# Kernel optimization log

Hardware: AMD Instinct MI355X
Metric: run time of the kernel (lower is better)

The kernel has to match this reference:

```python
import jax, jax.numpy as jnp
import numpy as np

B, L, DIM, S, K = 2, 2048, 1024, 16, 3
INNER = DIM  # expand = 1 (module only runs with expand=1, see notes)


def setup_inputs() -> dict:
    key = jax.random.key(0)
    ks = jax.random.split(key, 10)
    f = lambda k, shape, s=0.02: jax.random.normal(k, shape, jnp.float32) * s
    return {
        "x": jax.random.normal(ks[0], (B, L, DIM), jnp.float32),
        "gamma": jnp.ones((DIM,), jnp.float32),
        "beta": jnp.zeros((DIM,), jnp.float32),
        "W_in": f(ks[1], (2 * INNER, DIM)),
        "conv_w": f(ks[2], (INNER, 1, K), 0.2),   # depthwise conv, OIL layout
        "W_x": f(ks[3], (2 * S, INNER)),
        "W_dt": f(ks[4], (INNER, DIM)),
        "b_dt": f(ks[5], (INNER,), 0.1),
        "A_log": jax.random.normal(ks[6], (INNER, S), jnp.float32),
        "D_param": jnp.ones((INNER,), jnp.float32),
        "W_out": f(ks[7], (DIM, INNER)),
    }


def reference(x, gamma, beta, W_in, conv_w, W_x, W_dt, b_dt, A_log, D_param, W_out):
    residual = x
    # LayerNorm
    mu = jnp.mean(x, axis=-1, keepdims=True)
    var = jnp.var(x, axis=-1, keepdims=True)
    h = (x - mu) / jnp.sqrt(var + 1e-5) * gamma + beta
    # in_proj + chunk
    xz = jnp.einsum('bld,ed->ble', h, W_in)
    inner = W_in.shape[0] // 2
    xx, z = xz[..., :inner], xz[..., inner:]
    # depthwise conv1d, padding (K-1)//2, no bias
    k = conv_w.shape[-1]
    pad = (k - 1) // 2
    xc = jax.lax.conv_general_dilated(
        xx.transpose(0, 2, 1), conv_w, window_strides=(1,),
        padding=[(pad, pad)], dimension_numbers=('NCL', 'OIL', 'NCL'),
        feature_group_count=inner).transpose(0, 2, 1)
    xc = jax.nn.silu(xc)
    # projections for dt, B, C
    dt = jnp.einsum('bld,ed->ble', xc, W_dt) + b_dt
    BC = jnp.einsum('bld,ed->ble', xc, W_x)
    s = A_log.shape[-1]
    Bm, Cm = BC[..., :s], BC[..., s:]
    # selective scan
    A = -jnp.exp(A_log)                               # (d, s)
    dt = jax.nn.softplus(dt)                          # (b, l, d)
    dA = jnp.exp(jnp.einsum('bld,ds->blds', dt, A))   # (b, l, d, s)
    dB = jnp.einsum('bld,bls->blds', dt, Bm)          # (b, l, d, s)

    def step(state, inputs):
        dA_t, dB_t, C_t = inputs                      # (b,d,s), (b,d,s), (b,s)
        state = state * dA_t + dB_t
        y_t = jnp.einsum('bds,bs->bd', state, C_t)
        return state, y_t

    init = jnp.zeros((x.shape[0], inner, s), xc.dtype)
    _, ys = jax.lax.scan(
        step, init,
        (dA.transpose(1, 0, 2, 3), dB.transpose(1, 0, 2, 3), Cm.transpose(1, 0, 2)))
    y = ys.transpose(1, 0, 2)                         # (b, l, d)
    # skip, gate, out projection, residual
    y = y + D_param * xc
    y = y * jax.nn.silu(z)
    out = jnp.einsum('bld,ed->ble', y, W_out)
    return out + residual
```

## Files before the change

### kernel.cpp

```cpp
#include <hip/hip_runtime.h>
#include <math.h>

#define BB 2
#define LL 2048
#define DIMV 1024
#define SSV 16
#define INNERV 1024
#define E2V 2048
#define MMV (BB*LL)
#define NCHUNK 64
#define CLEN 32

typedef __attribute__((ext_vector_type(8))) short short8;
typedef __attribute__((ext_vector_type(4))) float f32x4;

static __device__ __forceinline__ float4 ld4(const float* p){
  return *reinterpret_cast<const float4*>(p);
}
static __device__ __forceinline__ ushort f2bf(float x){
  unsigned u = __float_as_uint(x);
  unsigned r = (u + 0x7fffu + ((u >> 16) & 1u)) >> 16;
  return (ushort)r;
}
static __device__ __forceinline__ float bf2f(ushort h){
  return __uint_as_float(((unsigned)h) << 16);
}
static __device__ __forceinline__ void gld16(const void* g, void* l){
  __builtin_amdgcn_global_load_lds(
      (const __attribute__((address_space(1))) void*)g,
      (__attribute__((address_space(3))) void*)l, 16, 0, 0);
}

__global__ __launch_bounds__(256) void ln_init(
        const float* __restrict__ x, const float* __restrict__ gamma,
        const float* __restrict__ beta, ushort* __restrict__ hh,
        const float* __restrict__ W_in, const float* __restrict__ W_dt,
        const float* __restrict__ W_out, const float* __restrict__ wx,
        ushort* __restrict__ Wih, ushort* __restrict__ Wdh,
        ushort* __restrict__ Woh, float* __restrict__ wxt){
  __shared__ float red[8];
  if (blockIdx.x < 4224){
    int idx = blockIdx.x*256 + threadIdx.x;
    if (idx < 1024*1024){
      const float* src; ushort* dst; int i;
      if (idx < 512*1024){ src = W_in;  dst = Wih; i = idx; }
      else if (idx < 768*1024){ src = W_dt;  dst = Wdh; i = idx - 512*1024; }
      else { src = W_out; dst = Woh; i = idx - 768*1024; }
      float4 v = ld4(src + (size_t)i*4);
      ushort4 H;
      H.x=f2bf(v.x); H.y=f2bf(v.y); H.z=f2bf(v.z); H.w=f2bf(v.w);
      *reinterpret_cast<ushort4*>(dst + (size_t)i*4) = H;
    } else {
      int j = idx - 1024*1024;
      int e = j >> 10, k = j & 1023;
      wxt[k*32 + e] = wx[j];
    }
    return;
  }
  int row = blockIdx.x - 4224;
  int tid = threadIdx.x;
  const float* xr = x + (size_t)row*DIMV;
  float4 v = ld4(xr + tid*4);
  float s  = v.x+v.y+v.z+v.w;
  float s2 = v.x*v.x+v.y*v.y+v.z*v.z+v.w*v.w;
  for (int o=32;o;o>>=1){ s += __shfl_down(s,o); s2 += __shfl_down(s2,o); }
  int wid = tid>>6, lane = tid&63;
  if (lane==0){ red[wid]=s; red[4+wid]=s2; }
  __syncthreads();
  s  = red[0]+red[1]+red[2]+red[3];
  s2 = red[4]+red[5]+red[6]+red[7];
  float mu  = s*(1.f/DIMV);
  float var = s2*(1.f/DIMV) - mu*mu;
  float rstd = rsqrtf(var + 1e-5f);
  float4 g = ld4(gamma + tid*4), be = ld4(beta + tid*4);
  ushort4 H;
  H.x = f2bf((v.x-mu)*rstd*g.x + be.x);
  H.y = f2bf((v.y-mu)*rstd*g.y + be.y);
  H.z = f2bf((v.z-mu)*rstd*g.z + be.z);
  H.w = f2bf((v.w-mu)*rstd*g.w + be.w);
  *reinterpret_cast<ushort4*>(hh + (size_t)row*DIMV + tid*4) = H;
}

#define GBK 64
#define NKT 16

template<int EPI, int BN>
__global__ __launch_bounds__(256) void gemm_bf16(
    const ushort* __restrict__ A, const ushort* __restrict__ Bw,
    void* __restrict__ Co_, int N, const float* __restrict__ aux){
  __shared__ __align__(16) ushort lds[(128+BN)*GBK];
  const int t  = threadIdx.x;
  const int bm = blockIdx.y * 128, bn = blockIdx.x * BN;

  const int rr  = t >> 3;
  const int k16 = (t & 7) ^ (rr & 7);
  const ushort* gA = A  + (size_t)(bm + rr)*1024 + k16*8;
  const ushort* gB = Bw + (size_t)(bn + rr)*1024 + k16*8;
  const int wofs = (t >> 6) * 1024;

  const int l  = t & 63, wv = t >> 6;
  const int wm = wv & 1, wn = wv >> 1;
  const int fr = l & 15, kb = l >> 4;
  const int WN = BN/2;
  const int NF = BN/64;

  f32x4 acc[4][2*NF];
  #pragma unroll
  for (int m=0;m<4;m++){
    #pragma unroll
    for (int n=0;n<2*NF;n++) acc[m][n] = (f32x4){0.f,0.f,0.f,0.f};
  }

  char* Lb = (char*)lds;
  for (int kt = 0; kt < NKT; ++kt){
    const int ko = kt*GBK;
    gld16(gA + ko,           Lb +     0 + wofs);
    gld16(gA + ko + 32*1024, Lb +  4096 + wofs);
    gld16(gA + ko + 64*1024, Lb +  8192 + wofs);
    gld16(gA + ko + 96*1024, Lb + 12288 + wofs);
    gld16(gB + ko,           Lb + 16384 + wofs);
    gld16(gB + ko + 32*1024, Lb + 20480 + wofs);
    if (BN == 128){
      gld16(gB + ko + 64*1024, Lb + 24576 + wofs);
      gld16(gB + ko + 96*1024, Lb + 28672 + wofs);
    }
    __syncthreads();
    short8 a[4][2], b[2*NF][2];
    #pragma unroll
    for (int m=0;m<4;m++){
      int row = wm*64 + m*16 + fr;
      #pragma unroll
      for (int ks=0;ks<2;ks++)
        a[m][ks] = *(const short8*)(Lb + row*128 + (((ks*4+kb)^(fr&7))*16));
    }
    #pragma unroll
    for (int n=0;n<2*NF;n++){
      int row = wn*WN + n*16 + fr;
      #pragma unroll
      for (int ks=0;ks<2;ks++)
        b[n][ks] = *(const short8*)(Lb + 16384 + row*128 + (((ks*4+kb)^(fr&7))*16));
    }
    #pragma unroll
    for (int ks=0;ks<2;ks++){
      #pragma unroll
      for (int m=0;m<4;m++){
        #pragma unroll
        for (int n=0;n<2*NF;n++)
          acc[m][n] = __builtin_amdgcn_mfma_f32_16x16x32_bf16(a[m][ks], b[n][ks], acc[m][n], 0,0,0);
      }
    }
    __syncthreads();
  }

  #pragma unroll
  for (int m=0;m<4;m++){
    int row0 = bm + wm*64 + m*16 + kb*4;
    #pragma unroll
    for (int n=0;n<2*NF;n++){
      int col = bn + wn*WN + n*16 + fr;
      #pragma unroll
      for (int j=0;j<4;j++){
        int r = row0 + j;
        float v = acc[m][n][j];
        if (EPI==0){
          ((ushort*)Co_)[(size_t)r*N + col] = f2bf(v);
        } else if (EPI==1){
          v += aux[col];
          v = (v > 20.f) ? v : log1pf(__expf(v));
          ((ushort*)Co_)[(size_t)r*N + col] = f2bf(v);
        } else {
          v += aux[(size_t)r*N + col];
          ((float*)Co_)[(size_t)r*N + col] = v;
        }
      }
    }
  }
}

__global__ __launch_bounds__(256) void bc_kernel(const ushort* __restrict__ xch,
        const float* __restrict__ wxt, float* __restrict__ bc){
  __shared__ ushort sh[8*1024];
  __shared__ float  sw[128*32];
  int tid = threadIdx.x;
  int row0 = blockIdx.x * 8;
  const ushort4* srcH = (const ushort4*)(xch + (size_t)row0*DIMV);
  #pragma unroll
  for (int i=0;i<8;i++)
    ((ushort4*)sh)[tid + i*256] = srcH[tid + i*256];
  int r = tid >> 5, e = tid & 31;
  float a0=0.f, a1=0.f, a2=0.f, a3=0.f;
  for (int kt=0; kt<8; ++kt){
    __syncthreads();
    const float4* wsrc = (const float4*)(wxt + kt*128*32);
    #pragma unroll
    for (int i=0;i<4;i++)
      ((float4*)sw)[tid + i*256] = wsrc[tid + i*256];
    __syncthreads();
    const ushort* xr = &sh[r*1024 + kt*128];
    #pragma unroll
    for (int k=0;k<128;k+=4){
      ushort4 xv = *(const ushort4*)&xr[k];
      a0 = fmaf(bf2f(xv.x), sw[(k+0)*32+e], a0);
      a1 = fmaf(bf2f(xv.y), sw[(k+1)*32+e], a1);
      a2 = fmaf(bf2f(xv.z), sw[(k+2)*32+e], a2);
      a3 = fmaf(bf2f(xv.w), sw[(k+3)*32+e], a3);
    }
  }
  bc[(size_t)(row0 + r)*32 + e] = (a0+a1)+(a2+a3);
}

__global__ __launch_bounds__(256) void conv_silu_kernel(const ushort* __restrict__ xz,
        const float* __restrict__ cw, ushort* __restrict__ xch){
  int idx = blockIdx.x*256 + threadIdx.x;
  int d4  = idx & 255;
  int row = idx >> 8;
  int t = row & (LL-1);
  const ushort* p = xz + (size_t)row*E2V + d4*4;
  ushort4 u1 = *reinterpret_cast<const ushort4*>(p);
  ushort4 u0 = (t>0)    ? *reinterpret_cast<const ushort4*>(p - E2V) : make_ushort4(0,0,0,0);
  ushort4 u2 = (t<LL-1) ? *reinterpret_cast<const ushort4*>(p + E2V) : make_ushort4(0,0,0,0);
  int d = d4*4;
  float w[12];
  #pragma unroll
  for (int i=0;i<12;i++) w[i] = cw[d*3 + i];
  float4 o;
  o.x = bf2f(u0.x)*w[0] + bf2f(u1.x)*w[1]  + bf2f(u2.x)*w[2];
  o.y = bf2f(u0.y)*w[3] + bf2f(u1.y)*w[4]  + bf2f(u2.y)*w[5];
  o.z = bf2f(u0.z)*w[6] + bf2f(u1.z)*w[7]  + bf2f(u2.z)*w[8];
  o.w = bf2f(u0.w)*w[9] + bf2f(u1.w)*w[10] + bf2f(u2.w)*w[11];
  o.x = o.x / (1.f + __expf(-o.x));
  o.y = o.y / (1.f + __expf(-o.y));
  o.z = o.z / (1.f + __expf(-o.z));
  o.w = o.w / (1.f + __expf(-o.w));
  ushort4 H;
  H.x=f2bf(o.x); H.y=f2bf(o.y); H.z=f2bf(o.z); H.w=f2bf(o.w);
  *reinterpret_cast<ushort4*>(xch + (size_t)row*DIMV + d4*4) = H;
}

__global__ __launch_bounds__(256) void scan_p1(const ushort* __restrict__ dt,
        const float* __restrict__ bc, const float* __restrict__ A_log,
        float* __restrict__ F, float* __restrict__ P){
  __shared__ float sB[CLEN*32];
  int bid = blockIdx.x;
  int dblk = bid & 3;
  int c  = (bid >> 2) & (NCHUNK-1);
  int b  = bid >> 8;
  int tid = threadIdx.x;
  int d = dblk*256 + tid;
  int row0 = b*LL + c*CLEN;
  ((float4*)sB)[tid] = *((const float4*)(bc + (size_t)row0*32) + tid);
  float a[16];
  {
    const float4* ap = (const float4*)(A_log + d*16);
    #pragma unroll
    for (int q=0;q<4;q++){
      float4 v = ap[q];
      a[q*4+0]=-__expf(v.x); a[q*4+1]=-__expf(v.y);
      a[q*4+2]=-__expf(v.z); a[q*4+3]=-__expf(v.w);
    }
  }
  __syncthreads();
  float st[16];
  #pragma unroll
  for (int s=0;s<16;s++) st[s]=0.f;
  float sdt = 0.f;
  const ushort* dtp = dt + (size_t)row0*DIMV + d;
  for (int t=0;t<CLEN;t++){
    float dtv = bf2f(dtp[(size_t)t*DIMV]);
    sdt += dtv;
    float4 B0 = *(const float4*)&sB[t*32+0];
    float4 B1 = *(const float4*)&sB[t*32+4];
    float4 B2 = *(const float4*)&sB[t*32+8];
    float4 B3 = *(const float4*)&sB[t*32+12];
    float Bv[16] = {B0.x,B0.y,B0.z,B0.w,B1.x,B1.y,B1.z,B1.w,
                    B2.x,B2.y,B2.z,B2.w,B3.x,B3.y,B3.z,B3.w};
    #pragma unroll
    for (int s=0;s<16;s++){
      float dA = __expf(dtv*a[s]);
      st[s] = fmaf(st[s], dA, dtv*Bv[s]);
    }
  }
  size_t o = ((size_t)((b*NCHUNK + c)*DIMV + d))*16;
  #pragma unroll
  for (int q=0;q<4;q++){
    *(float4*)(F + o + q*4) = make_float4(st[q*4],st[q*4+1],st[q*4+2],st[q*4+3]);
    *(float4*)(P + o + q*4) = make_float4(__expf(sdt*a[q*4]),  __expf(sdt*a[q*4+1]),
                                          __expf(sdt*a[q*4+2]),__expf(sdt*a[q*4+3]));
  }
}

__global__ __launch_bounds__(256) void scan_p2(const float* __restrict__ F,
        const float* __restrict__ P, float* __restrict__ E){
  int idx = blockIdx.x*256 + threadIdx.x;
  int b  = idx >> 14;
  int ds = idx & 16383;
  float e = 0.f;
  for (int c=0;c<NCHUNK;c++){
    size_t o = ((size_t)(b*NCHUNK + c) << 14) + ds;
    E[o] = e;
    e = fmaf(P[o], e, F[o]);
  }
}

__global__ __launch_bounds__(256) void scan_p3(const ushort* __restrict__ dt,
        const float* __restrict__ bc, const float* __restrict__ A_log,
        const float* __restrict__ E, const ushort* __restrict__ xch,
        const ushort* __restrict__ xz, const float* __restrict__ Dp,
        ushort* __restrict__ yh){
  __shared__ float sBC[CLEN*32];
  int bid = blockIdx.x;
  int dblk = bid & 3;
  int c  = (bid >> 2) & (NCHUNK-1);
  int b  = bid >> 8;
  int tid = threadIdx.x;
  int d = dblk*256 + tid;
  int row0 = b*LL + c*CLEN;
  ((float4*)sBC)[tid] = *((const float4*)(bc + (size_t)row0*32) + tid);
  float a[16];
  {
    const float4* ap = (const float4*)(A_log + d*16);
    #pragma unroll
    for (int q=0;q<4;q++){
      float4 v = ap[q];
      a[q*4+0]=-__expf(v.x); a[q*4+1]=-__expf(v.y);
      a[q*4+2]=-__expf(v.z); a[q*4+3]=-__expf(v.w);
    }
  }
  float st[16];
  {
    size_t o = ((size_t)((b*NCHUNK + c)*DIMV + d))*16;
    #pragma unroll
    for (int q=0;q<4;q++){
      float4 v = *(const float4*)(E + o + q*4);
      st[q*4]=v.x; st[q*4+1]=v.y; st[q*4+2]=v.z; st[q*4+3]=v.w;
    }
  }
  float Dv = Dp[d];
  __syncthreads();
  const ushort* dtp = dt + (size_t)row0*DIMV + d;
  for (int t=0;t<CLEN;t++){
    float dtv = bf2f(dtp[(size_t)t*DIMV]);
    float4 B0 = *(const float4*)&sBC[t*32+0];
    float4 B1 = *(const float4*)&sBC[t*32+4];
    float4 B2 = *(const float4*)&sBC[t*32+8];
    float4 B3 = *(const float4*)&sBC[t*32+12];
    float4 C0 = *(const float4*)&sBC[t*32+16];
    float4 C1 = *(const float4*)&sBC[t*32+20];
    float4 C2 = *(const float4*)&sBC[t*32+24];
    float4 C3 = *(const float4*)&sBC[t*32+28];
    float Bv[16] = {B0.x,B0.y,B0.z,B0.w,B1.x,B1.y,B1.z,B1.w,
                    B2.x,B2.y,B2.z,B2.w,B3.x,B3.y,B3.z,B3.w};
    float Cv[16] = {C0.x,C0.y,C0.z,C0.w,C1.x,C1.y,C1.z,C1.w,
                    C2.x,C2.y,C2.z,C2.w,C3.x,C3.y,C3.z,C3.w};
    float y = 0.f;
    #pragma unroll
    for (int s=0;s<16;s++){
      float dA = __expf(dtv*a[s]);
      st[s] = fmaf(st[s], dA, dtv*Bv[s]);
      y = fmaf(st[s], Cv[s], y);
    }
    int row = row0 + t;
    size_t ofs = (size_t)row*DIMV + d;
    float xcv = bf2f(xch[ofs]);
    float zv  = bf2f(xz[(size_t)row*E2V + INNERV + d]);
    float sz  = zv / (1.f + __expf(-zv));
    yh[ofs] = f2bf((y + Dv*xcv)*sz);
  }
}

extern "C" void kernel_launch(void* const* d_in, const int* in_sizes, int n_in,
                              void* d_out, int out_size, void* d_ws, size_t ws_size,
                              hipStream_t stream){
  const float* x     = (const float*)d_in[0];
  const float* gamma = (const float*)d_in[1];
  const float* beta  = (const float*)d_in[2];
  const float* W_in  = (const float*)d_in[3];
  const float* cw    = (const float*)d_in[4];
  const float* W_x   = (const float*)d_in[5];
  const float* W_dt  = (const float*)d_in[6];
  const float* b_dt  = (const float*)d_in[7];
  const float* A_log = (const float*)d_in[8];
  const float* Dp    = (const float*)d_in[9];
  const float* W_out = (const float*)d_in[10];
  float* out = (float*)d_out;
  float* ws  = (float*)d_ws;
  const size_t MB = (size_t)1 << 20;
  ushort* xzh = (ushort*)ws;
  ushort* hh  = (ushort*)(ws + 4*MB);
  ushort* yh  = (ushort*)(ws + 4*MB);
  ushort* xch = (ushort*)(ws + 6*MB);
  ushort* dtb = (ushort*)(ws + 8*MB);
  float*  F   = ws + 10*MB;
  float*  P   = ws + 12*MB;
  float*  E   = ws + 14*MB;
  ushort* Wih = (ushort*)(ws + 16*MB);
  ushort* Wdh = (ushort*)(ws + 17*MB);
  ushort* Woh = (ushort*)(ws + 17*MB + 512*1024);
  float*  bcb = ws + 18*MB;
  float*  wxt = ws + 18*MB + 128*1024;

  ln_init<<<4224 + MMV, 256, 0, stream>>>(x, gamma, beta, hh,
                                          W_in, W_dt, W_out, W_x,
                                          Wih, Wdh, Woh, wxt);
  gemm_bf16<0,128><<<dim3(E2V/128, MMV/128), 256, 0, stream>>>(hh, Wih, xzh, E2V, nullptr);
  conv_silu_kernel<<<(MMV*(DIMV/4))/256, 256, 0, stream>>>(xzh, cw, xch);
  gemm_bf16<1,64><<<dim3(INNERV/64, MMV/128), 256, 0, stream>>>(xch, Wdh, dtb, INNERV, b_dt);
  bc_kernel<<<MMV/8, 256, 0, stream>>>(xch, wxt, bcb);
  scan_p1<<<BB*NCHUNK*(DIMV/256), 256, 0, stream>>>(dtb, bcb, A_log, F, P);
  scan_p2<<<(BB*DIMV*SSV)/256, 256, 0, stream>>>(F, P, E);
  scan_p3<<<BB*NCHUNK*(DIMV/256), 256, 0, stream>>>(dtb, bcb, A_log, E, xch, xzh, Dp, yh);
  gemm_bf16<2,64><<<dim3(DIMV/64, MMV/128), 256, 0, stream>>>(yh, Woh, out, DIMV, x);
}
```

Before: 167.7 us.

## Split in_proj, fuse z-GEMM with dt-GEMM and BC into one launch; bf16 scan states

The in_proj GEMM is split so only the x half runs before the conv. The z half, the dt projection GEMM and the B/C projection are merged into one heterogeneous kernel, dispatched by block index, to fill the GPU and cut launches. Separately, the chunk-scan intermediates F, P and E are stored as bf16 instead of fp32, halving their traffic. This costs accuracy in the carried scan state and exp-decay products, and LDS use in the merged kernel is sized for the largest branch.

```diff
diff --git a/kernel.cpp b/kernel.cpp
--- a/kernel.cpp
+++ b/kernel.cpp
@@ -85,13 +85,11 @@
 #define NKT 16
 
 template<int EPI, int BN>
-__global__ __launch_bounds__(256) void gemm_bf16(
+static __device__ __forceinline__ void gemm_body(ushort* lds,
     const ushort* __restrict__ A, const ushort* __restrict__ Bw,
-    void* __restrict__ Co_, int N, const float* __restrict__ aux){
-  __shared__ __align__(16) ushort lds[(128+BN)*GBK];
+    void* __restrict__ Co_, int N, const float* __restrict__ aux,
+    int bm, int bn){
   const int t  = threadIdx.x;
-  const int bm = blockIdx.y * 128, bn = blockIdx.x * BN;
-
   const int rr  = t >> 3;
   const int k16 = (t & 7) ^ (rr & 7);
   const ushort* gA = A  + (size_t)(bm + rr)*1024 + k16*8;
@@ -177,12 +175,19 @@
   }
 }
 
-__global__ __launch_bounds__(256) void bc_kernel(const ushort* __restrict__ xch,
-        const float* __restrict__ wxt, float* __restrict__ bc){
-  __shared__ ushort sh[8*1024];
-  __shared__ float  sw[128*32];
+template<int EPI, int BN>
+__global__ __launch_bounds__(256) void gemm_bf16(
+    const ushort* __restrict__ A, const ushort* __restrict__ Bw,
+    void* __restrict__ Co_, int N, const float* __restrict__ aux){
+  __shared__ __align__(16) ushort lds[(128+BN)*GBK];
+  gemm_body<EPI,BN>(lds, A, Bw, Co_, N, aux, blockIdx.y*128, blockIdx.x*BN);
+}
+
+static __device__ __forceinline__ void bc_body(ushort* sh, float* sw,
+    const ushort* __restrict__ xch, const float* __restrict__ wxt,
+    float* __restrict__ bc, int blk){
   int tid = threadIdx.x;
-  int row0 = blockIdx.x * 8;
+  int row0 = blk * 8;
   const ushort4* srcH = (const ushort4*)(xch + (size_t)row0*DIMV);
   #pragma unroll
   for (int i=0;i<8;i++)
@@ -209,16 +214,34 @@
   bc[(size_t)(row0 + r)*32 + e] = (a0+a1)+(a2+a3);
 }
 
-__global__ __launch_bounds__(256) void conv_silu_kernel(const ushort* __restrict__ xz,
+__global__ __launch_bounds__(256) void fused_mid(
+    const ushort* __restrict__ hh, const ushort* __restrict__ Wz,
+    ushort* __restrict__ zh,
+    const ushort* __restrict__ xch, const ushort* __restrict__ Wdh,
+    ushort* __restrict__ dtb, const float* __restrict__ b_dt,
+    const float* __restrict__ wxt, float* __restrict__ bcb){
+  __shared__ __align__(16) ushort lds[16384];
+  int bid = blockIdx.x;
+  if (bid < 256){
+    gemm_body<0,128>(lds, hh, Wz, zh, DIMV, nullptr, (bid>>3)*128, (bid&7)*128);
+  } else if (bid < 768){
+    int t2 = bid - 256;
+    gemm_body<1,64>(lds, xch, Wdh, dtb, INNERV, b_dt, (t2>>4)*128, (t2&15)*64);
+  } else {
+    bc_body(lds, (float*)(lds + 8192), xch, wxt, bcb, bid - 768);
+  }
+}
+
+__global__ __launch_bounds__(256) void conv_silu_kernel(const ushort* __restrict__ xxh,
         const float* __restrict__ cw, ushort* __restrict__ xch){
   int idx = blockIdx.x*256 + threadIdx.x;
   int d4  = idx & 255;
   int row = idx >> 8;
   int t = row & (LL-1);
-  const ushort* p = xz + (size_t)row*E2V + d4*4;
+  const ushort* p = xxh + (size_t)row*DIMV + d4*4;
   ushort4 u1 = *reinterpret_cast<const ushort4*>(p);
-  ushort4 u0 = (t>0)    ? *reinterpret_cast<const ushort4*>(p - E2V) : make_ushort4(0,0,0,0);
-  ushort4 u2 = (t<LL-1) ? *reinterpret_cast<const ushort4*>(p + E2V) : make_ushort4(0,0,0,0);
+  ushort4 u0 = (t>0)    ? *reinterpret_cast<const ushort4*>(p - DIMV) : make_ushort4(0,0,0,0);
+  ushort4 u2 = (t<LL-1) ? *reinterpret_cast<const ushort4*>(p + DIMV) : make_ushort4(0,0,0,0);
   int d = d4*4;
   float w[12];
   #pragma unroll
@@ -239,7 +262,7 @@
 
 __global__ __launch_bounds__(256) void scan_p1(const ushort* __restrict__ dt,
         const float* __restrict__ bc, const float* __restrict__ A_log,
-        float* __restrict__ F, float* __restrict__ P){
+        ushort* __restrict__ F, ushort* __restrict__ P){
   __shared__ float sB[CLEN*32];
   int bid = blockIdx.x;
   int dblk = bid & 3;
@@ -283,29 +306,33 @@
   size_t o = ((size_t)((b*NCHUNK + c)*DIMV + d))*16;
   #pragma unroll
   for (int q=0;q<4;q++){
-    *(float4*)(F + o + q*4) = make_float4(st[q*4],st[q*4+1],st[q*4+2],st[q*4+3]);
-    *(float4*)(P + o + q*4) = make_float4(__expf(sdt*a[q*4]),  __expf(sdt*a[q*4+1]),
-                                          __expf(sdt*a[q*4+2]),__expf(sdt*a[q*4+3]));
-  }
-}
-
-__global__ __launch_bounds__(256) void scan_p2(const float* __restrict__ F,
-        const float* __restrict__ P, float* __restrict__ E){
+    ushort4 fv, pv;
+    fv.x=f2bf(st[q*4]);   fv.y=f2bf(st[q*4+1]);
+    fv.z=f2bf(st[q*4+2]); fv.w=f2bf(st[q*4+3]);
+    pv.x=f2bf(__expf(sdt*a[q*4]));   pv.y=f2bf(__expf(sdt*a[q*4+1]));
+    pv.z=f2bf(__expf(sdt*a[q*4+2])); pv.w=f2bf(__expf(sdt*a[q*4+3]));
+    *(ushort4*)(F + o + q*4) = fv;
+    *(ushort4*)(P + o + q*4) = pv;
+  }
+}
+
+__global__ __launch_bounds__(256) void scan_p2(const ushort* __restrict__ F,
+        const ushort* __restrict__ P, ushort* __restrict__ E){
   int idx = blockIdx.x*256 + threadIdx.x;
   int b  = idx >> 14;
   int ds = idx & 16383;
   float e = 0.f;
   for (int c=0;c<NCHUNK;c++){
     size_t o = ((size_t)(b*NCHUNK + c) << 14) + ds;
-    E[o] = e;
-    e = fmaf(P[o], e, F[o]);
+    E[o] = f2bf(e);
+    e = fmaf(bf2f(P[o]), e, bf2f(F[o]));
   }
 }
 
 __global__ __launch_bounds__(256) void scan_p3(const ushort* __restrict__ dt,
         const float* __restrict__ bc, const float* __restrict__ A_log,
-        const float* __restrict__ E, const ushort* __restrict__ xch,
-        const ushort* __restrict__ xz, const float* __restrict__ Dp,
+        const ushort* __restrict__ E, const ushort* __restrict__ xch,
+        const ushort* __restrict__ zh, const float* __restrict__ Dp,
         ushort* __restrict__ yh){
   __shared__ float sBC[CLEN*32];
   int bid = blockIdx.x;
@@ -331,8 +358,8 @@
     size_t o = ((size_t)((b*NCHUNK + c)*DIMV + d))*16;
     #pragma unroll
     for (int q=0;q<4;q++){
-      float4 v = *(const float4*)(E + o + q*4);
-      st[q*4]=v.x; st[q*4+1]=v.y; st[q*4+2]=v.z; st[q*4+3]=v.w;
+      ushort4 v = *(const ushort4*)(E + o + q*4);
+      st[q*4]=bf2f(v.x); st[q*4+1]=bf2f(v.y); st[q*4+2]=bf2f(v.z); st[q*4+3]=bf2f(v.w);
     }
   }
   float Dv = Dp[d];
@@ -362,7 +389,7 @@
     int row = row0 + t;
     size_t ofs = (size_t)row*DIMV + d;
     float xcv = bf2f(xch[ofs]);
-    float zv  = bf2f(xz[(size_t)row*E2V + INNERV + d]);
+    float zv  = bf2f(zh[ofs]);
     float sz  = zv / (1.f + __expf(-zv));
     yh[ofs] = f2bf((y + Dv*xcv)*sz);
   }
@@ -385,29 +412,30 @@
   float* out = (float*)d_out;
   float* ws  = (float*)d_ws;
   const size_t MB = (size_t)1 << 20;
-  ushort* xzh = (ushort*)ws;
+  ushort* xxh = (ushort*)ws;
+  ushort* zh  = (ushort*)(ws + 2*MB);
   ushort* hh  = (ushort*)(ws + 4*MB);
   ushort* yh  = (ushort*)(ws + 4*MB);
   ushort* xch = (ushort*)(ws + 6*MB);
   ushort* dtb = (ushort*)(ws + 8*MB);
-  float*  F   = ws + 10*MB;
-  float*  P   = ws + 12*MB;
-  float*  E   = ws + 14*MB;
-  ushort* Wih = (ushort*)(ws + 16*MB);
-  ushort* Wdh = (ushort*)(ws + 17*MB);
-  ushort* Woh = (ushort*)(ws + 17*MB + 512*1024);
-  float*  bcb = ws + 18*MB;
-  float*  wxt = ws + 18*MB + 128*1024;
+  ushort* F   = (ushort*)(ws + 10*MB);
+  ushort* P   = (ushort*)(ws + 11*MB);
+  ushort* E   = (ushort*)(ws + 12*MB);
+  ushort* Wih = (ushort*)(ws + 13*MB);
+  ushort* Wdh = (ushort*)(ws + 14*MB);
+  ushort* Woh = (ushort*)(ws + 14*MB + 512*1024);
+  float*  bcb = ws + 15*MB;
+  float*  wxt = ws + 15*MB + 128*1024;
 
   ln_init<<<4224 + MMV, 256, 0, stream>>>(x, gamma, beta, hh,
                                           W_in, W_dt, W_out, W_x,
                                           Wih, Wdh, Woh, wxt);
-  gemm_bf16<0,128><<<dim3(E2V/128, MMV/128), 256, 0, stream>>>(hh, Wih, xzh, E2V, nullptr);
-  conv_silu_kernel<<<(MMV*(DIMV/4))/256, 256, 0, stream>>>(xzh, cw, xch);
-  gemm_bf16<1,64><<<dim3(INNERV/64, MMV/128), 256, 0, stream>>>(xch, Wdh, dtb, INNERV, b_dt);
-  bc_kernel<<<MMV/8, 256, 0, stream>>>(xch, wxt, bcb);
+  gemm_bf16<0,128><<<dim3(8, MMV/128), 256, 0, stream>>>(hh, Wih, xxh, DIMV, nullptr);
+  conv_silu_kernel<<<(MMV*(DIMV/4))/256, 256, 0, stream>>>(xxh, cw, xch);
+  fused_mid<<<1280, 256, 0, stream>>>(hh, Wih + (size_t)1024*1024, zh,
+                                      xch, Wdh, dtb, b_dt, wxt, bcb);
   scan_p1<<<BB*NCHUNK*(DIMV/256), 256, 0, stream>>>(dtb, bcb, A_log, F, P);
   scan_p2<<<(BB*DIMV*SSV)/256, 256, 0, stream>>>(F, P, E);
-  scan_p3<<<BB*NCHUNK*(DIMV/256), 256, 0, stream>>>(dtb, bcb, A_log, E, xch, xzh, Dp, yh);
+  scan_p3<<<BB*NCHUNK*(DIMV/256), 256, 0, stream>>>(dtb, bcb, A_log, E, xch, zh, Dp, yh);
   gemm_bf16<2,64><<<dim3(DIMV/64, MMV/128), 256, 0, stream>>>(yh, Woh, out, DIMV, x);
 }
```

New measurement: 181.6 us. +8.3%, slower.
